# Performance work log

Measured on AMD Instinct MI355X. Metric: run time of the kernel, lower is better.

## Reference

```python
import jax, jax.numpy as jnp
import numpy as np

# UMAP a,b fitted offline for spread=5, min_dist=0.001 (curve_fit of 1/(1+a x^(2b)))
ALPHA = 0.1520
BETA = 0.7900
N_NODES = 50000
IN_DIM = 128
HID = 64
OUT_DIM = 2
N_EDGES = 800000


def setup_inputs() -> dict:
    key = jax.random.key(0)
    ks = jax.random.split(key, 8)
    feats = jax.random.normal(ks[0], (N_NODES, IN_DIM), dtype=jnp.float32)
    W1 = jax.random.normal(ks[1], (IN_DIM, HID), dtype=jnp.float32) / np.sqrt(IN_DIM)
    b1 = jnp.zeros((HID,), dtype=jnp.float32)
    W2 = jax.random.normal(ks[2], (HID, OUT_DIM), dtype=jnp.float32) / np.sqrt(HID)
    b2 = jnp.zeros((OUT_DIM,), dtype=jnp.float32)
    edge_index = jax.random.randint(ks[3], (2, N_EDGES), 0, N_NODES, dtype=jnp.int64)
    row_neg = jax.random.randint(ks[4], (N_EDGES,), 0, N_NODES, dtype=jnp.int64)
    col_neg = jax.random.randint(ks[5], (N_EDGES,), 0, N_NODES, dtype=jnp.int64)
    return {"features": feats, "W1": W1, "b1": b1, "W2": W2, "b2": b2,
            "edge_index": edge_index, "row_neg": row_neg, "col_neg": col_neg}


def _gcn_norm(edge_index, n_nodes):
    # add self-loops, symmetric normalization D^-1/2 (A+I) D^-1/2
    loops = jnp.arange(n_nodes, dtype=edge_index.dtype)
    row = jnp.concatenate([edge_index[0], loops])
    col = jnp.concatenate([edge_index[1], loops])
    deg = jax.ops.segment_sum(jnp.ones_like(row, dtype=jnp.float32), row,
                              num_segments=n_nodes)
    dinv = jnp.where(deg > 0, jax.lax.rsqrt(deg), 0.0)
    norm = dinv[row] * dinv[col]  # [E + N]
    return row, col, norm


def _gcn_conv(x, W, b, row, col, norm, n_nodes):
    h = x @ W                      # [N, out]
    msg = h[col] * norm[:, None]   # edge-indexed gather (irregular access)
    agg = jax.ops.segment_sum(msg, row, num_segments=n_nodes)
    return agg + b


def _forward(features, W1, b1, W2, b2, edge_index, row_neg, col_neg):
    n = features.shape[0]
    row, col, norm = _gcn_norm(edge_index, n)
    h = jax.nn.relu(_gcn_conv(features, W1, b1, row, col, norm, n))
    emb = _gcn_conv(h, W2, b2, row, col, norm, n)  # [N, 2]
    # pairwise L2 distances at positive edges and negative samples
    pos_diff = emb[edge_index[0]] - emb[edge_index[1]]
    neg_diff = emb[row_neg] - emb[col_neg]
    eps = 1e-12  # guards grad at zero distance (torch.norm subgradient is 0 there)
    pos_d = jnp.sqrt(jnp.sum(pos_diff * pos_diff, axis=1) + eps)
    neg_d = jnp.sqrt(jnp.sum(neg_diff * neg_diff, axis=1) + eps)
    lowdim_dist = jnp.concatenate([pos_d, neg_d], axis=0)  # [2E]
    q = 1.0 / (1.0 + ALPHA * jnp.power(lowdim_dist, 2.0 * BETA))
    return emb, q


def reference(features, W1, b1, W2, b2, edge_index, row_neg, col_neg):
    return _forward(features, W1, b1, W2, b2, edge_index, row_neg, col_neg)
```

## Files before the change

### kernel.cpp

```cpp
#include <hip/hip_runtime.h>
#include <hip/hip_fp16.h>
#include <math.h>

constexpr int   NN     = 50000;
constexpr int   IN_DIM = 128;
constexpr int   HID    = 64;
constexpr int   NE     = 800000;
constexpr float ALPHA  = 0.1520f;
constexpr float BETA   = 0.7900f;

constexpr int RSH = 7;
constexpr int RPB = 1 << RSH;
constexpr int NB  = (NN + RPB - 1) / RPB;
constexpr int NBP = 512;
constexpr int CH  = 4096;
constexpr int NCH = (NE + CH - 1) / CH;
constexpr int CAP = 4096;

__global__ __launch_bounds__(256) void k_bhist(const int* __restrict__ row,
                                               int* __restrict__ bhist) {
    __shared__ int h[NBP];
    int t = threadIdx.x;
    for (int i = t; i < NBP; i += 256) h[i] = 0;
    __syncthreads();
    int e0 = blockIdx.x * CH;
#pragma unroll
    for (int i = 0; i < 16; ++i) {
        int e = e0 + i * 256 + t;
        if (e < NE) atomicAdd(&h[row[e] >> RSH], 1);
    }
    __syncthreads();
    for (int b = t; b < NB; b += 256)
        if (h[b]) atomicAdd(&bhist[b], h[b]);
}

__global__ void k_bscan(const int* __restrict__ bhist, int* __restrict__ boffs,
                        int* __restrict__ bcur) {
    __shared__ int s[NBP];
    int t = threadIdx.x;
    s[t]       = (t < NB) ? bhist[t] : 0;
    s[t + 256] = (t + 256 < NB) ? bhist[t + 256] : 0;
    __syncthreads();
    for (int d = 1; d < NBP; d <<= 1) {
        int v0 = (t >= d) ? s[t - d] : 0;
        int v1 = (t + 256 >= d) ? s[t + 256 - d] : 0;
        __syncthreads();
        s[t] += v0;
        s[t + 256] += v1;
        __syncthreads();
    }
    if (t < NB)       { int e = s[t] - bhist[t];             boffs[t] = e;       bcur[t] = e; }
    if (t + 256 < NB) { int e = s[t + 256] - bhist[t + 256]; boffs[t + 256] = e; bcur[t + 256] = e; }
    if (t == 0) boffs[NB] = NE;
}

__global__ __launch_bounds__(256) void k_binfill(const int* __restrict__ row,
                                                 const int* __restrict__ col,
                                                 int* __restrict__ bcur,
                                                 unsigned int* __restrict__ bedge) {
    __shared__ int hist[NBP];
    __shared__ int scn[NBP];
    __shared__ int ebase[NB];
    __shared__ int gbase[NB];
    __shared__ int lcur[NB];
    __shared__ unsigned int pk[CH];
    __shared__ int gof[CH];

    int t = threadIdx.x;
    int e0 = blockIdx.x * CH;
    int rw[16], cl[16];
#pragma unroll
    for (int i = 0; i < 16; ++i) {
        int e = e0 + i * 256 + t;
        if (e < NE) { rw[i] = row[e]; cl[i] = col[e]; } else rw[i] = -1;
    }
    for (int i = t; i < NBP; i += 256) hist[i] = 0;
    __syncthreads();
#pragma unroll
    for (int i = 0; i < 16; ++i)
        if (rw[i] >= 0) atomicAdd(&hist[rw[i] >> RSH], 1);
    __syncthreads();
    scn[t] = hist[t];
    scn[t + 256] = hist[t + 256];
    __syncthreads();
    for (int d = 1; d < NBP; d <<= 1) {
        int v0 = (t >= d) ? scn[t - d] : 0;
        int v1 = (t + 256 >= d) ? scn[t + 256 - d] : 0;
        __syncthreads();
        scn[t] += v0;
        scn[t + 256] += v1;
        __syncthreads();
    }
    for (int b = t; b < NB; b += 256) {
        int h  = hist[b];
        int eb = scn[b] - h;
        ebase[b] = eb;
        lcur[b]  = eb;
        gbase[b] = h ? atomicAdd(&bcur[b], h) : 0;
    }
    __syncthreads();
#pragma unroll
    for (int i = 0; i < 16; ++i) {
        if (rw[i] >= 0) {
            int b = rw[i] >> RSH;
            int s = atomicAdd(&lcur[b], 1);
            pk[s]  = ((unsigned int)(rw[i] & (RPB - 1)) << 17) | (unsigned int)cl[i];
            gof[s] = gbase[b] + (s - ebase[b]);
        }
    }
    __syncthreads();
    int nval = min(CH, NE - e0);
    for (int s = t; s < nval; s += 256) bedge[gof[s]] = pk[s];
}

__global__ __launch_bounds__(256) void k_bucket(const unsigned int* __restrict__ bedge,
                                                const int* __restrict__ boffs,
                                                int* __restrict__ offs,
                                                float* __restrict__ dinv,
                                                int* __restrict__ scol) {
    __shared__ int cnt[RPB];
    __shared__ int loff[RPB];
    __shared__ int wtot[2];
    __shared__ unsigned int ld[CAP];
    __shared__ int buf[CAP];

    int b = blockIdx.x, t = threadIdx.x;
    int beg = boffs[b], end = boffs[b + 1];
    int m = end - beg;
    int nbase = b << RSH;

    if (t < RPB) cnt[t] = 0;
    __syncthreads();

    if (m <= CAP) {
        for (int i = t; i < m; i += 256) {
            unsigned int mm = bedge[beg + i];
            ld[i] = mm;
            atomicAdd(&cnt[mm >> 17], 1);
        }
        __syncthreads();
        if (t < RPB) {
            int v = cnt[t];
            int x = v;
#pragma unroll
            for (int d = 1; d < 64; d <<= 1) {
                int y = __shfl_up(x, d);
                if ((t & 63) >= d) x += y;
            }
            if ((t & 63) == 63) wtot[t >> 6] = x;
            loff[t] = x - v;
        }
        __syncthreads();
        if (t >= 64 && t < RPB) loff[t] += wtot[0];
        __syncthreads();
        if (t < RPB) {
            int n = nbase + t;
            if (n < NN) {
                offs[n] = beg + loff[t];
                dinv[n] = rsqrtf((float)(cnt[t] + 1));
            }
        }
        if (b == NB - 1 && t == 0) offs[NN] = NE;
        if (t < RPB) cnt[t] = loff[t];
        __syncthreads();
        for (int i = t; i < m; i += 256) {
            unsigned int mm = ld[i];
            int s = atomicAdd(&cnt[mm >> 17], 1);
            buf[s] = (int)(mm & 0x1FFFFu);
        }
        __syncthreads();
        for (int i = t; i < m; i += 256) scol[beg + i] = buf[i];
    } else {
        for (int i = t; i < m; i += 256)
            atomicAdd(&cnt[bedge[beg + i] >> 17], 1);
        __syncthreads();
        if (t < RPB) {
            int v = cnt[t];
            int x = v;
#pragma unroll
            for (int d = 1; d < 64; d <<= 1) {
                int y = __shfl_up(x, d);
                if ((t & 63) >= d) x += y;
            }
            if ((t & 63) == 63) wtot[t >> 6] = x;
            loff[t] = x - v;
        }
        __syncthreads();
        if (t >= 64 && t < RPB) loff[t] += wtot[0];
        __syncthreads();
        if (t < RPB) {
            int n = nbase + t;
            if (n < NN) {
                offs[n] = beg + loff[t];
                dinv[n] = rsqrtf((float)(cnt[t] + 1));
            }
        }
        if (b == NB - 1 && t == 0) offs[NN] = NE;
        if (t < RPB) cnt[t] = loff[t];
        __syncthreads();
        for (int i = t; i < m; i += 256) {
            unsigned int mm = bedge[beg + i];
            int s = atomicAdd(&cnt[mm >> 17], 1);
            scol[beg + s] = (int)(mm & 0x1FFFFu);
        }
    }
}

__global__ __launch_bounds__(256) void k_gemm1(const float* __restrict__ feat,
                                               const float* __restrict__ W1,
                                               const float* __restrict__ dinv,
                                               __half* __restrict__ h1s) {
    __shared__ float sW[IN_DIM * HID];
    __shared__ float sF[16][IN_DIM];
    int t = threadIdx.x;

    const float4* W4  = (const float4*)W1;
    float4*       sW4 = (float4*)sW;
#pragma unroll
    for (int i = 0; i < 8; ++i) sW4[t + i * 256] = W4[t + i * 256];

    int n0 = blockIdx.x * 16;
    const float4* F4  = (const float4*)(feat + (size_t)n0 * IN_DIM);
    float4*       sF4 = (float4*)&sF[0][0];
    sF4[t]       = F4[t];
    sF4[t + 256] = F4[t + 256];
    __syncthreads();

    int c = t & 63;
    int g = t >> 6;
    float acc[4] = {0.f, 0.f, 0.f, 0.f};
    for (int k = 0; k < IN_DIM; ++k) {
        float w = sW[k * HID + c];
#pragma unroll
        for (int i = 0; i < 4; ++i) acc[i] += sF[g * 4 + i][k] * w;
    }
#pragma unroll
    for (int i = 0; i < 4; ++i) {
        int n = n0 + g * 4 + i;
        h1s[(size_t)n * HID + c] = __float2half(acc[i] * dinv[n]);
    }
}

__global__ __launch_bounds__(256) void k_agg1(const int* __restrict__ offs,
                                              const int* __restrict__ scol,
                                              const float* __restrict__ dinv,
                                              const __half* __restrict__ h1s,
                                              const float* __restrict__ b1,
                                              const float* __restrict__ W2,
                                              float* __restrict__ h2s) {
    int n    = blockIdx.x * 4 + (threadIdx.x >> 6);
    int lane = threadIdx.x & 63;
    if (n >= NN) return;
    int beg = offs[n], end = offs[n + 1];
    float acc = 0.f;
    int k = beg;
    for (; k + 3 < end; k += 4) {
        int c0 = scol[k], c1 = scol[k + 1], c2 = scol[k + 2], c3 = scol[k + 3];
        float v0 = __half2float(h1s[(size_t)c0 * HID + lane]);
        float v1 = __half2float(h1s[(size_t)c1 * HID + lane]);
        float v2 = __half2float(h1s[(size_t)c2 * HID + lane]);
        float v3 = __half2float(h1s[(size_t)c3 * HID + lane]);
        acc += (v0 + v1) + (v2 + v3);
    }
    for (; k < end; ++k)
        acc += __half2float(h1s[(size_t)scol[k] * HID + lane]);

    float di = dinv[n];
    acc = di * (acc + __half2float(h1s[(size_t)n * HID + lane]));
    acc += b1[lane];
    acc = fmaxf(acc, 0.f);
    float p0 = acc * W2[lane * 2 + 0];
    float p1 = acc * W2[lane * 2 + 1];
#pragma unroll
    for (int d = 32; d >= 1; d >>= 1) {
        p0 += __shfl_xor(p0, d);
        p1 += __shfl_xor(p1, d);
    }
    if (lane == 0) {
        h2s[(size_t)n * 2 + 0] = di * p0;
        h2s[(size_t)n * 2 + 1] = di * p1;
    }
}

__global__ __launch_bounds__(256) void k_agg2(const int* __restrict__ offs,
                                              const int* __restrict__ scol,
                                              const float* __restrict__ dinv,
                                              const float* __restrict__ h2s,
                                              const float* __restrict__ b2,
                                              float* __restrict__ emb) {
    int n    = blockIdx.x * 4 + (threadIdx.x >> 6);
    int lane = threadIdx.x & 63;
    if (n >= NN) return;
    int beg = offs[n], end = offs[n + 1];
    float e0 = 0.f, e1 = 0.f;
    const float2* h22 = (const float2*)h2s;
    for (int k = beg + lane; k < end; k += 64) {
        float2 v = h22[scol[k]];
        e0 += v.x;
        e1 += v.y;
    }
#pragma unroll
    for (int d = 32; d >= 1; d >>= 1) {
        e0 += __shfl_xor(e0, d);
        e1 += __shfl_xor(e1, d);
    }
    if (lane == 0) {
        float di = dinv[n];
        float2 self = h22[n];
        emb[(size_t)n * 2 + 0] = di * (e0 + self.x) + b2[0];
        emb[(size_t)n * 2 + 1] = di * (e1 + self.y) + b2[1];
    }
}

__global__ void k_q(const int* __restrict__ pr, const int* __restrict__ pc,
                    const int* __restrict__ nr, const int* __restrict__ nc,
                    const float* __restrict__ emb, float* __restrict__ q) {
    int e = blockIdx.x * blockDim.x + threadIdx.x;
    if (e >= 2 * NE) return;
    int a, b;
    if (e < NE) { a = pr[e]; b = pc[e]; }
    else        { a = nr[e - NE]; b = nc[e - NE]; }
    const float2* e2 = (const float2*)emb;
    float2 A = e2[a], B = e2[b];
    float dx = A.x - B.x, dy = A.y - B.y;
    float d = sqrtf(dx * dx + dy * dy + 1e-12f);
    float p = exp2f(2.0f * BETA * log2f(d));
    q[e] = 1.0f / (1.0f + ALPHA * p);
}

extern "C" void kernel_launch(void* const* d_in, const int* in_sizes, int n_in,
                              void* d_out, int out_size, void* d_ws, size_t ws_size,
                              hipStream_t stream) {
    const float* feat = (const float*)d_in[0];
    const float* W1   = (const float*)d_in[1];
    const float* b1   = (const float*)d_in[2];
    const float* W2   = (const float*)d_in[3];
    const float* b2   = (const float*)d_in[4];
    const int*   ei   = (const int*)d_in[5];
    const int*   nrw  = (const int*)d_in[6];
    const int*   ncl  = (const int*)d_in[7];
    const int* row = ei;
    const int* col = ei + NE;

    char* cur = (char*)d_ws;
    auto alloc = [&](size_t bytes) -> char* {
        char* p = cur;
        cur += (bytes + 255) & ~(size_t)255;
        return p;
    };
    int*          bhist = (int*)alloc(sizeof(int) * NB);
    int*          boffs = (int*)alloc(sizeof(int) * (NB + 1));
    int*          bcur  = (int*)alloc(sizeof(int) * NB);
    int*          offs  = (int*)alloc(sizeof(int) * (NN + 1));
    float*        dinv  = (float*)alloc(sizeof(float) * NN);
    unsigned int* bedge = (unsigned int*)alloc(sizeof(unsigned int) * NE);
    int*          scol  = (int*)alloc(sizeof(int) * NE);
    float*        h2s   = (float*)alloc(sizeof(float) * (size_t)NN * 2);
    __half*       h1s   = (__half*)alloc(sizeof(__half) * (size_t)NN * HID);

    float* emb = (float*)d_out;
    float* q   = (float*)d_out + (size_t)NN * 2;

    hipError_t _e = hipMemsetAsync(bhist, 0, sizeof(int) * NB, stream);
    (void)_e;

    k_bhist  <<<NCH, 256, 0, stream>>>(row, bhist);
    k_bscan  <<<1, 256, 0, stream>>>(bhist, boffs, bcur);
    k_binfill<<<NCH, 256, 0, stream>>>(row, col, bcur, bedge);
    k_bucket <<<NB, 256, 0, stream>>>(bedge, boffs, offs, dinv, scol);

    k_gemm1<<<NN / 16, 256, 0, stream>>>(feat, W1, dinv, h1s);

    k_agg1<<<(NN + 3) / 4, 256, 0, stream>>>(offs, scol, dinv, h1s, b1, W2, h2s);
    k_agg2<<<(NN + 3) / 4, 256, 0, stream>>>(offs, scol, dinv, h2s, b2, emb);

    k_q<<<(2 * NE + 255) / 256, 256, 0, stream>>>(row, col, nrw, ncl, emb, q);
}
```

Measured before the change: 128.3 us.

## Vectorize agg1 gathers, pack 4 nodes per wave in agg2, drop histogram atomics

k_agg1 now has each wave split into four 16-lane groups. Each group processes a different neighbor and loads 8-byte half4 vectors, replacing the scalar half loads, and the groups are combined with cross-lane shuffles. k_agg2 assigns 16 lanes per node, so average-degree nodes no longer leave most of a 64-lane wave idle. The bucket histogram writes per-chunk partial counts that a new reduction kernel sums, which removes the global atomics and the memset at the cost of one extra launch.

```diff
diff --git a/kernel.cpp b/kernel.cpp
--- a/kernel.cpp
+++ b/kernel.cpp
@@ -18,7 +18,7 @@
 constexpr int CAP = 4096;
 
 __global__ __launch_bounds__(256) void k_bhist(const int* __restrict__ row,
-                                               int* __restrict__ bhist) {
+                                               int* __restrict__ bpart) {
     __shared__ int h[NBP];
     int t = threadIdx.x;
     for (int i = t; i < NBP; i += 256) h[i] = 0;
@@ -30,8 +30,16 @@
         if (e < NE) atomicAdd(&h[row[e] >> RSH], 1);
     }
     __syncthreads();
-    for (int b = t; b < NB; b += 256)
-        if (h[b]) atomicAdd(&bhist[b], h[b]);
+    for (int b = t; b < NB; b += 256) bpart[b * NCH + blockIdx.x] = h[b];
+}
+
+__global__ void k_bsum(const int* __restrict__ bpart, int* __restrict__ bhist) {
+    int b = blockIdx.x;
+    int v = 0;
+    for (int i = threadIdx.x; i < NCH; i += 64) v += bpart[b * NCH + i];
+#pragma unroll
+    for (int d = 32; d >= 1; d >>= 1) v += __shfl_xor(v, d);
+    if (threadIdx.x == 0) bhist[b] = v;
 }
 
 __global__ void k_bscan(const int* __restrict__ bhist, int* __restrict__ boffs,
@@ -251,28 +259,52 @@
     int n    = blockIdx.x * 4 + (threadIdx.x >> 6);
     int lane = threadIdx.x & 63;
     if (n >= NN) return;
+    int g  = lane >> 4;
+    int cq = lane & 15;
     int beg = offs[n], end = offs[n + 1];
-    float acc = 0.f;
-    int k = beg;
-    for (; k + 3 < end; k += 4) {
-        int c0 = scol[k], c1 = scol[k + 1], c2 = scol[k + 2], c3 = scol[k + 3];
-        float v0 = __half2float(h1s[(size_t)c0 * HID + lane]);
-        float v1 = __half2float(h1s[(size_t)c1 * HID + lane]);
-        float v2 = __half2float(h1s[(size_t)c2 * HID + lane]);
-        float v3 = __half2float(h1s[(size_t)c3 * HID + lane]);
-        acc += (v0 + v1) + (v2 + v3);
-    }
-    for (; k < end; ++k)
-        acc += __half2float(h1s[(size_t)scol[k] * HID + lane]);
-
+
+    const uint2* H = (const uint2*)h1s;
+    float a0 = 0.f, a1 = 0.f, a2 = 0.f, a3 = 0.f;
+    int k = beg + g;
+    for (; k + 4 < end; k += 8) {
+        uint2 va = H[(size_t)scol[k] * 16 + cq];
+        uint2 vb = H[(size_t)scol[k + 4] * 16 + cq];
+        float2 fa0 = __half22float2(*(__half2*)&va.x);
+        float2 fa1 = __half22float2(*(__half2*)&va.y);
+        float2 fb0 = __half22float2(*(__half2*)&vb.x);
+        float2 fb1 = __half22float2(*(__half2*)&vb.y);
+        a0 += fa0.x + fb0.x;
+        a1 += fa0.y + fb0.y;
+        a2 += fa1.x + fb1.x;
+        a3 += fa1.y + fb1.y;
+    }
+    if (k < end) {
+        uint2 va = H[(size_t)scol[k] * 16 + cq];
+        float2 fa0 = __half22float2(*(__half2*)&va.x);
+        float2 fa1 = __half22float2(*(__half2*)&va.y);
+        a0 += fa0.x; a1 += fa0.y; a2 += fa1.x; a3 += fa1.y;
+    }
+    a0 += __shfl_xor(a0, 16); a0 += __shfl_xor(a0, 32);
+    a1 += __shfl_xor(a1, 16); a1 += __shfl_xor(a1, 32);
+    a2 += __shfl_xor(a2, 16); a2 += __shfl_xor(a2, 32);
+    a3 += __shfl_xor(a3, 16); a3 += __shfl_xor(a3, 32);
+
+    uint2 sv = H[(size_t)n * 16 + cq];
+    float2 s0 = __half22float2(*(__half2*)&sv.x);
+    float2 s1 = __half22float2(*(__half2*)&sv.y);
     float di = dinv[n];
-    acc = di * (acc + __half2float(h1s[(size_t)n * HID + lane]));
-    acc += b1[lane];
-    acc = fmaxf(acc, 0.f);
-    float p0 = acc * W2[lane * 2 + 0];
-    float p1 = acc * W2[lane * 2 + 1];
-#pragma unroll
-    for (int d = 32; d >= 1; d >>= 1) {
+    float4 b14 = ((const float4*)b1)[cq];
+    a0 = fmaxf(di * (a0 + s0.x) + b14.x, 0.f);
+    a1 = fmaxf(di * (a1 + s0.y) + b14.y, 0.f);
+    a2 = fmaxf(di * (a2 + s1.x) + b14.z, 0.f);
+    a3 = fmaxf(di * (a3 + s1.y) + b14.w, 0.f);
+
+    float4 w01 = ((const float4*)W2)[cq * 2];
+    float4 w23 = ((const float4*)W2)[cq * 2 + 1];
+    float p0 = a0 * w01.x + a1 * w01.z + a2 * w23.x + a3 * w23.z;
+    float p1 = a0 * w01.y + a1 * w01.w + a2 * w23.y + a3 * w23.w;
+#pragma unroll
+    for (int d = 8; d >= 1; d >>= 1) {
         p0 += __shfl_xor(p0, d);
         p1 += __shfl_xor(p1, d);
     }
@@ -288,23 +320,25 @@
                                               const float* __restrict__ h2s,
                                               const float* __restrict__ b2,
                                               float* __restrict__ emb) {
-    int n    = blockIdx.x * 4 + (threadIdx.x >> 6);
+    int wid  = threadIdx.x >> 6;
     int lane = threadIdx.x & 63;
-    if (n >= NN) return;
-    int beg = offs[n], end = offs[n + 1];
+    int n = blockIdx.x * 16 + wid * 4 + (lane >> 4);
+    int e = lane & 15;
+    const float2* h22 = (const float2*)h2s;
     float e0 = 0.f, e1 = 0.f;
-    const float2* h22 = (const float2*)h2s;
-    for (int k = beg + lane; k < end; k += 64) {
+    int beg = 0, end = 0;
+    if (n < NN) { beg = offs[n]; end = offs[n + 1]; }
+    for (int k = beg + e; k < end; k += 16) {
         float2 v = h22[scol[k]];
         e0 += v.x;
         e1 += v.y;
     }
 #pragma unroll
-    for (int d = 32; d >= 1; d >>= 1) {
+    for (int d = 8; d >= 1; d >>= 1) {
         e0 += __shfl_xor(e0, d);
         e1 += __shfl_xor(e1, d);
     }
-    if (lane == 0) {
+    if (e == 0 && n < NN) {
         float di = dinv[n];
         float2 self = h22[n];
         emb[(size_t)n * 2 + 0] = di * (e0 + self.x) + b2[0];
@@ -348,6 +382,7 @@
         cur += (bytes + 255) & ~(size_t)255;
         return p;
     };
+    int*          bpart = (int*)alloc(sizeof(int) * (size_t)NB * NCH);
     int*          bhist = (int*)alloc(sizeof(int) * NB);
     int*          boffs = (int*)alloc(sizeof(int) * (NB + 1));
     int*          bcur  = (int*)alloc(sizeof(int) * NB);
@@ -361,10 +396,8 @@
     float* emb = (float*)d_out;
     float* q   = (float*)d_out + (size_t)NN * 2;
 
-    hipError_t _e = hipMemsetAsync(bhist, 0, sizeof(int) * NB, stream);
-    (void)_e;
-
-    k_bhist  <<<NCH, 256, 0, stream>>>(row, bhist);
+    k_bhist  <<<NCH, 256, 0, stream>>>(row, bpart);
+    k_bsum   <<<NB, 64, 0, stream>>>(bpart, bhist);
     k_bscan  <<<1, 256, 0, stream>>>(bhist, boffs, bcur);
     k_binfill<<<NCH, 256, 0, stream>>>(row, col, bcur, bedge);
     k_bucket <<<NB, 256, 0, stream>>>(bedge, boffs, offs, dinv, scol);
@@ -372,7 +405,7 @@
     k_gemm1<<<NN / 16, 256, 0, stream>>>(feat, W1, dinv, h1s);
 
     k_agg1<<<(NN + 3) / 4, 256, 0, stream>>>(offs, scol, dinv, h1s, b1, W2, h2s);
-    k_agg2<<<(NN + 3) / 4, 256, 0, stream>>>(offs, scol, dinv, h2s, b2, emb);
+    k_agg2<<<(NN + 15) / 16, 256, 0, stream>>>(offs, scol, dinv, h2s, b2, emb);
 
     k_q<<<(2 * NE + 255) / 256, 256, 0, stream>>>(row, col, nrw, ncl, emb, q);
 }
```

New measurement: 107.8 us. -16.0%, faster.
